# Optimization experiments

Measured on AMD Instinct MI355X. Metric: run time of the kernel, lower is better.

Reference implementation:

```python
import jax, jax.numpy as jnp
import numpy as np

PI = 3.141592653589793
TAU = 2.0      # tau for both rpe_lif (spikingjelly default 2.0) and act_conv (params['tau'])
V_TH = 1.0     # spikingjelly LIFNode default v_threshold
EPS = 1e-5     # LayerNorm / BatchNorm eps


@jax.custom_vjp
def atan_spike(x):
    # Heaviside forward, ATan surrogate backward (spikingjelly surrogate.ATan, alpha=2)
    return (x >= 0.0).astype(x.dtype)

def _atan_fwd(x):
    return atan_spike(x), x

def _atan_bwd(x, g):
    # (alpha/2) / (1 + ((pi/2)*alpha*x)^2) with alpha=2 -> 1/(1+(pi*x)^2)
    return (g / (1.0 + (PI * x) ** 2),)

atan_spike.defvjp(_atan_fwd, _atan_bwd)


def lif(x_seq, tau=TAU):
    """Multi-step LIF: decay_input=True, v_reset=0, hard reset, detach_reset.
    x_seq: [T, ...]; returns spikes [T, ...]."""
    def step(v, x):
        v = v + (x - v) / tau                      # neuronal charge
        s = atan_spike(v - V_TH)                   # fire
        v = v * (1.0 - jax.lax.stop_gradient(s))   # detached hard reset to 0
        return v, s
    _, spikes = jax.lax.scan(step, jnp.zeros_like(x_seq[0]), x_seq)
    return spikes


def setup_inputs() -> dict:
    key = jax.random.key(0)
    ks = jax.random.split(key, 8)
    B, L, D, T = 256, 50, 128, 4
    n_items, n_h, n_v = 100001, 8, 4
    emb = jax.random.normal(ks[0], (n_items, D), jnp.float32) * 0.5
    emb = emb.at[0].set(0.0)  # padding_idx=0
    return {
        "item_seq": jax.random.randint(ks[1], (B, L), 0, n_items, jnp.int32),
        "emb_table": emb,
        "ln_gamma": jnp.ones((D,), jnp.float32),
        "ln_beta": jnp.zeros((D,), jnp.float32),
        "conv_v_w": jax.random.normal(ks[2], (n_v, L), jnp.float32) * float(1.0 / np.sqrt(L)),
        # per-length kernels stored padded: kernel for length k=i+1 is conv_h_w[i, :, :k, :]
        "conv_h_w": jax.random.normal(ks[3], (L, n_h, L, D), jnp.float32) * 0.02,
        "bn_gamma": jnp.ones((L, n_h), jnp.float32),
        "bn_beta": jnp.zeros((L, n_h), jnp.float32),
        "fc_h_w": jax.random.normal(ks[4], (D, n_h * L), jnp.float32) * 0.05,
        "fc_h_b": jnp.zeros((D,), jnp.float32),
        "fc_v_w": jax.random.normal(ks[5], (D, n_v * D), jnp.float32) * 0.04,
        "fc_v_b": jnp.zeros((D,), jnp.float32),
        "T": 4,
    }


def reference(item_seq, emb_table, ln_gamma, ln_beta, conv_v_w, conv_h_w,
              bn_gamma, bn_beta, fc_h_w, fc_h_b, fc_v_w, fc_v_b, T):
    B, L = item_seq.shape
    D = emb_table.shape[1]
    n_h = conv_h_w.shape[1]
    n_v = conv_v_w.shape[0]

    # embedding + LayerNorm
    emb = emb_table[item_seq]                                   # [B,L,D]
    mu = emb.mean(-1, keepdims=True)
    var = emb.var(-1, keepdims=True)
    x = (emb - mu) / jnp.sqrt(var + EPS) * ln_gamma + ln_beta   # [B,L,D]

    # repeat over T and spike (rpe_lif)
    s = lif(jnp.broadcast_to(x, (T, B, L, D)))                  # binary spikes [T,B,L,D]

    # vertical conv: kernel (L,1), no bias -> collapses seq axis
    out_v = jnp.einsum('tbld,cl->tbcd', s, conv_v_w).reshape(T, B, n_v * D)

    # horizontal multi-scale convs + BN(train stats) + LIF + global max pool
    s2 = s.reshape(T * B, 1, L, D)
    pools = []
    for i in range(L):
        k = i + 1
        w = conv_h_w[i, :, :k, :][:, None]                      # [n_h,1,k,D]
        y = jax.lax.conv_general_dilated(
            s2, w, (1, 1), 'VALID',
            dimension_numbers=('NCHW', 'OIHW', 'NCHW'))[:, :, :, 0]  # [TB,n_h,L-k+1]
        m = y.mean(axis=(0, 2))                                  # BN over (T*B, spatial)
        v = y.var(axis=(0, 2))
        y = (y - m[:, None]) * (bn_gamma[i][:, None] / jnp.sqrt(v[:, None] + EPS)) + bn_beta[i][:, None]
        y = lif(y.reshape(T, B, n_h, L - k + 1))                 # [T,B,n_h,L-k+1]
        pools.append(y.max(axis=-1))                             # [T,B,n_h]
    out_h = jnp.concatenate(pools, axis=-1)                      # [T,B,n_h*L]

    out_h = (out_h @ fc_h_w.T + fc_h_b).mean(0)                  # [B,D]
    out_v = out_v.mean(0) @ fc_v_w.T + fc_v_b                    # [B,D]
    return out_h + out_v
```

## Files before the change

### kernel.cpp

```cpp
#include <hip/hip_runtime.h>

#define B_ 256
#define L_ 50
#define D_ 128
#define T_ 4
#define NH 8
#define NV 4
#define TB_ (T_*B_)
#define EPSF 1e-5f

typedef _Float16 h8 __attribute__((ext_vector_type(8)));
typedef float f4 __attribute__((ext_vector_type(4)));

typedef __attribute__((address_space(1))) const unsigned int gas_u32;
typedef __attribute__((address_space(3))) unsigned int las_u32;
#define GLOAD_LDS16(gp, lp) __builtin_amdgcn_global_load_lds((gas_u32*)(gp), (las_u32*)(lp), 16, 0, 0)

__device__ __forceinline__ float waveSum(float v) {
    #pragma unroll
    for (int o = 32; o > 0; o >>= 1) v += __shfl_down(v, o, 64);
    return v;
}

__device__ __forceinline__ size_t yoff(int i) {
    return (size_t)8192 * (size_t)(50 * i - (i * (i - 1)) / 2);
}

__global__ __launch_bounds__(256) void k0_wsplit(
        const float* __restrict__ w, _Float16* __restrict__ whl) {
    int dk = blockIdx.x, i = blockIdx.y;
    int t = threadIdx.x;
    int c = t >> 4, gd = t & 15;
    int h = c & 7;
    bool live = (i < 50) && (dk <= i);
    const float* src = w + (((size_t)i * NH + h) * L_ + dk) * D_ + gd * 8;
    h8 o;
    #pragma unroll
    for (int e = 0; e < 8; ++e) {
        float wv = live ? src[e] : 0.f;
        _Float16 hi = (_Float16)wv;
        o[e] = (c < 8) ? hi : (_Float16)((wv - (float)hi) * 1024.f);
    }
    *(h8*)(whl + (((size_t)i * 50 + dk) * 16 + c) * 128 + ((gd ^ c) & 15) * 8) = o;
}

__global__ __launch_bounds__(128) void k1_embed_ln_lif(
        const int* __restrict__ item, const float* __restrict__ tab,
        const float* __restrict__ g, const float* __restrict__ be,
        _Float16* __restrict__ s16, float* __restrict__ smean) {
    int bid = blockIdx.x;
    int b = bid / L_, l = bid % L_;
    int d = threadIdx.x;
    int wid = d >> 6, lane = d & 63;
    __shared__ float red[2];
    int it = item[b * L_ + l];
    float e = tab[(size_t)it * D_ + d];
    float sm_ = waveSum(e);
    if (lane == 0) red[wid] = sm_;
    __syncthreads();
    float mu = (red[0] + red[1]) * (1.f / 128.f);
    __syncthreads();
    float df = e - mu;
    float s2 = waveSum(df * df);
    if (lane == 0) red[wid] = s2;
    __syncthreads();
    float var = (red[0] + red[1]) * (1.f / 128.f);
    float x = df / sqrtf(var + EPSF) * g[d] + be[d];
    float v = 0.f, acc = 0.f;
    int pos = (((d >> 3) ^ l) & 15) * 8 + (d & 7);
    #pragma unroll
    for (int t = 0; t < T_; ++t) {
        v += (x - v) * 0.5f;
        float sp = (v >= 1.f) ? 1.f : 0.f;
        v *= (1.f - sp);
        s16[((size_t)(t * B_ + b) * L_ + l) * D_ + pos] = (_Float16)sp;
        acc += sp;
    }
    smean[((size_t)b * L_ + l) * D_ + d] = acc * 0.25f;
}

template<int MTG>
__global__ __launch_bounds__(256, 1) void k2a(
        const _Float16* __restrict__ s16, const _Float16* __restrict__ whl,
        float* __restrict__ y, int gbase) {
    extern __shared__ __align__(16) char lds[];
    char* bring = lds + 51200;
    const int tbq = blockIdx.x;
    const int grp = gbase + blockIdx.y;
    const int i0 = grp * 4;
    const int kmax = i0 + 4;
    const int tid = threadIdx.x;
    const int wave = tid >> 6, lane = tid & 63;
    const int c_ = lane & 15, g = lane >> 4;

    {
        const float4* src = (const float4*)(s16 + (size_t)tbq * 4 * (L_ * D_));
        float4* dst = (float4*)lds;
        for (int idx = tid; idx < 3200; idx += 256) dst[idx] = src[idx];
    }
    const char* bsrc = (const char*)(whl + ((size_t)(i0 + wave) * 50) * 2048);
    {
        #pragma unroll
        for (int s = 0; s < 5; ++s) {
            if (s < kmax) {
                const char* gp = bsrc + (size_t)s * 4096 + lane * 16;
                char* lp = bring + s * 16384 + wave * 4096 + lane * 16;
                #pragma unroll
                for (int q = 0; q < 4; ++q)
                    GLOAD_LDS16(gp + q * 1024, lp + q * 1024);
            }
        }
    }
    asm volatile("s_waitcnt lgkmcnt(0)" ::: "memory");
    __builtin_amdgcn_s_barrier();
    __builtin_amdgcn_sched_barrier(0);

    f4 acc[4][MTG];
    #pragma unroll
    for (int s = 0; s < 4; ++s)
        #pragma unroll
        for (int j = 0; j < MTG; ++j) { f4 z = {0.f, 0.f, 0.f, 0.f}; acc[s][j] = z; }

    const char* Abase = lds + wave * 12800;
    int boff[4];
    #pragma unroll
    for (int dc = 0; dc < 4; ++dc)
        boff[dc] = c_ * 256 + ((((dc << 2) + g) ^ c_) & 15) * 16;

    int rdpos = 0, wrpos = 81920;
    for (int dk = 0; dk < kmax; ++dk) {
        int ahead = kmax - 1 - dk; if (ahead > 4) ahead = 4;
        if (ahead >= 4)      asm volatile("s_waitcnt vmcnt(16)" ::: "memory");
        else if (ahead == 3) asm volatile("s_waitcnt vmcnt(12)" ::: "memory");
        else if (ahead == 2) asm volatile("s_waitcnt vmcnt(8)" ::: "memory");
        else if (ahead == 1) asm volatile("s_waitcnt vmcnt(4)" ::: "memory");
        else                 asm volatile("s_waitcnt vmcnt(0)" ::: "memory");
        __builtin_amdgcn_s_barrier();
        __builtin_amdgcn_sched_barrier(0);
        if (dk + 5 < kmax) {
            const char* gp = bsrc + (size_t)(dk + 5) * 4096 + lane * 16;
            char* lp = bring + wrpos + wave * 4096 + lane * 16;
            #pragma unroll
            for (int q = 0; q < 4; ++q)
                GLOAD_LDS16(gp + q * 1024, lp + q * 1024);
        }
        const char* Bs = bring + rdpos;
        #pragma unroll
        for (int dc = 0; dc < 4; ++dc) {
            h8 b0 = *(const h8*)(Bs + boff[dc]);
            h8 b1 = *(const h8*)(Bs + 4096 + boff[dc]);
            h8 b2 = *(const h8*)(Bs + 8192 + boff[dc]);
            h8 b3 = *(const h8*)(Bs + 12288 + boff[dc]);
            #pragma unroll
            for (int jt = 0; jt < MTG; ++jt) {
                int l = jt * 16 + c_ + dk; if (l > 49) l = 49;
                h8 a = *(const h8*)(Abase + l * 256 + ((((dc << 2) + g) ^ l) & 15) * 16);
                acc[0][jt] = __builtin_amdgcn_mfma_f32_16x16x32_f16(a, b0, acc[0][jt], 0, 0, 0);
                acc[1][jt] = __builtin_amdgcn_mfma_f32_16x16x32_f16(a, b1, acc[1][jt], 0, 0, 0);
                acc[2][jt] = __builtin_amdgcn_mfma_f32_16x16x32_f16(a, b2, acc[2][jt], 0, 0, 0);
                acc[3][jt] = __builtin_amdgcn_mfma_f32_16x16x32_f16(a, b3, acc[3][jt], 0, 0, 0);
            }
        }
        rdpos += 16384; if (rdpos == 98304) rdpos = 0;
        wrpos += 16384; if (wrpos == 98304) wrpos = 0;
    }
    const int tb = tbq * 4 + wave;
    const bool hiLane = (c_ < 8);
    const int h = c_ & 7;
    #pragma unroll
    for (int s = 0; s < 4; ++s) {
        const int i = i0 + s;
        const int J = 50 - i;
        size_t yb = yoff(i) + ((size_t)tb * NH + h) * J;
        #pragma unroll
        for (int jt = 0; jt < MTG; ++jt) {
            #pragma unroll
            for (int r = 0; r < 4; ++r) {
                float lo = __shfl_xor(acc[s][jt][r], 8, 64);
                int j = jt * 16 + g * 4 + r;
                if (hiLane && j < J) y[yb + j] = acc[s][jt][r] + lo * (1.f / 1024.f);
            }
        }
    }
}

__global__ __launch_bounds__(256, 1) void k2c(
        const _Float16* __restrict__ s16, const _Float16* __restrict__ whl,
        float* __restrict__ y) {
    extern __shared__ __align__(16) char lds[];
    char* bring = lds + 102400;
    const int tbo = blockIdx.x;
    const int i0 = 36 + blockIdx.y * 4;
    const int kmax = (i0 + 4 <= 50) ? (i0 + 4) : 50;
    const int tid = threadIdx.x;
    const int wave = tid >> 6, lane = tid & 63;
    const int tq = wave & 1, sg = wave >> 1;
    const int c_ = lane & 15, g = lane >> 4;

    {
        const float4* src = (const float4*)(s16 + (size_t)tbo * 8 * (L_ * D_));
        float4* dst = (float4*)lds;
        for (int idx = tid; idx < 6400; idx += 256) dst[idx] = src[idx];
    }
    const char* bsrc = (const char*)(whl + ((size_t)(i0 + wave) * 50) * 2048);
    {
        #pragma unroll
        for (int s = 0; s < 2; ++s) {
            const char* gp = bsrc + (size_t)s * 4096 + lane * 16;
            char* lp = bring + s * 16384 + wave * 4096 + lane * 16;
            #pragma unroll
            for (int q = 0; q < 4; ++q)
                GLOAD_LDS16(gp + q * 1024, lp + q * 1024);
        }
    }
    asm volatile("s_waitcnt lgkmcnt(0)" ::: "memory");
    __builtin_amdgcn_s_barrier();
    __builtin_amdgcn_sched_barrier(0);

    f4 acc[2][4];
    #pragma unroll
    for (int s = 0; s < 2; ++s)
        #pragma unroll
        for (int t = 0; t < 4; ++t) { f4 z = {0.f, 0.f, 0.f, 0.f}; acc[s][t] = z; }

    const char* Aq = lds + (tq * 4) * 12800;
    int boff[4];
    #pragma unroll
    for (int dc = 0; dc < 4; ++dc)
        boff[dc] = c_ * 256 + ((((dc << 2) + g) ^ c_) & 15) * 16;

    int rdpos = 0, wrpos = 32768;
    for (int dk = 0; dk < kmax; ++dk) {
        if (dk + 1 < kmax) asm volatile("s_waitcnt vmcnt(4)" ::: "memory");
        else               asm volatile("s_waitcnt vmcnt(0)" ::: "memory");
        __builtin_amdgcn_s_barrier();
        __builtin_amdgcn_sched_barrier(0);
        if (dk + 2 < kmax) {
            const char* gp = bsrc + (size_t)(dk + 2) * 4096 + lane * 16;
            char* lp = bring + wrpos + wave * 4096 + lane * 16;
            #pragma unroll
            for (int q = 0; q < 4; ++q)
                GLOAD_LDS16(gp + q * 1024, lp + q * 1024);
        }
        const char* Bs = bring + rdpos + sg * 8192;
        #pragma unroll
        for (int dc = 0; dc < 4; ++dc) {
            h8 b0 = *(const h8*)(Bs + boff[dc]);
            h8 b1 = *(const h8*)(Bs + 4096 + boff[dc]);
            int l = c_ + dk; if (l > 49) l = 49;
            int aoff = l * 256 + ((((dc << 2) + g) ^ l) & 15) * 16;
            #pragma unroll
            for (int tbL = 0; tbL < 4; ++tbL) {
                h8 a = *(const h8*)(Aq + tbL * 12800 + aoff);
                acc[0][tbL] = __builtin_amdgcn_mfma_f32_16x16x32_f16(a, b0, acc[0][tbL], 0, 0, 0);
                acc[1][tbL] = __builtin_amdgcn_mfma_f32_16x16x32_f16(a, b1, acc[1][tbL], 0, 0, 0);
            }
        }
        rdpos += 16384; if (rdpos == 49152) rdpos = 0;
        wrpos += 16384; if (wrpos == 49152) wrpos = 0;
    }
    const bool hiLane = (c_ < 8);
    const int h = c_ & 7;
    #pragma unroll
    for (int s = 0; s < 2; ++s) {
        const int i = i0 + sg * 2 + s;
        const int J = 50 - i;
        if (J <= 0) continue;
        #pragma unroll
        for (int tbL = 0; tbL < 4; ++tbL) {
            const int tb = tbo * 8 + tq * 4 + tbL;
            size_t yb = yoff(i) + ((size_t)tb * NH + h) * J;
            #pragma unroll
            for (int r = 0; r < 4; ++r) {
                float lo = __shfl_xor(acc[s][tbL][r], 8, 64);
                int j = g * 4 + r;
                if (hiLane && j < J) y[yb + j] = acc[s][tbL][r] + lo * (1.f / 1024.f);
            }
        }
    }
}

__global__ __launch_bounds__(256) void k3_partial(
        const float* __restrict__ y, float* __restrict__ psum) {
    int ih = blockIdx.x, ck = blockIdx.y;
    int i = ih >> 3, h = ih & 7;
    int J = 50 - i;
    size_t yb = yoff(i);
    int tid = threadIdx.x;
    int grp = tid >> 5, sub = tid & 31;
    float sm = 0.f, ss = 0.f;
    for (int tb = ck * 128 + grp; tb < (ck + 1) * 128; tb += 8) {
        const float* row = y + yb + ((size_t)tb * NH + h) * J;
        for (int j = sub; j < J; j += 32) { float v = row[j]; sm += v; ss += v * v; }
    }
    __shared__ float r1[4], r2[4];
    float a = waveSum(sm), b = waveSum(ss);
    int wid = tid >> 6, lane = tid & 63;
    if (lane == 0) { r1[wid] = a; r2[wid] = b; }
    __syncthreads();
    if (tid == 0) {
        psum[((size_t)ih * 8 + ck) * 2]     = r1[0] + r1[1] + r1[2] + r1[3];
        psum[((size_t)ih * 8 + ck) * 2 + 1] = r2[0] + r2[1] + r2[2] + r2[3];
    }
}

__global__ __launch_bounds__(256) void k3_final(
        const float* __restrict__ psum, const float* __restrict__ bng,
        float* __restrict__ statm, float* __restrict__ stats_) {
    int ih = blockIdx.x * 256 + threadIdx.x;
    if (ih >= 400) return;
    float S = 0.f, Q = 0.f;
    for (int ck = 0; ck < 8; ++ck) {
        S += psum[((size_t)ih * 8 + ck) * 2];
        Q += psum[((size_t)ih * 8 + ck) * 2 + 1];
    }
    int i = ih >> 3;
    float cnt = 1024.f * (float)(50 - i);
    float m = S / cnt;
    float var = Q / cnt - m * m; if (var < 0.f) var = 0.f;
    statm[ih] = m;
    stats_[ih] = bng[ih] / sqrtf(var + EPSF);
}

__global__ __launch_bounds__(512) void k4_bn_lif_pool(
        const float* __restrict__ y, const float* __restrict__ statm,
        const float* __restrict__ stats_, const float* __restrict__ bnb,
        float* __restrict__ ps) {
    int b = blockIdx.x, i = blockIdx.y, J = L_ - i;
    int h = threadIdx.x >> 6, lane = threadIdx.x & 63;
    int ih = i * NH + h;
    float m = statm[ih], sc = stats_[ih], bb = bnb[ih];
    size_t yb = yoff(i);
    bool valid = lane < J;
    float v = 0.f; int cnt = 0;
    #pragma unroll
    for (int t = 0; t < T_; ++t) {
        int tb = t * B_ + b;
        float yn;
        if (valid) {
            float raw = y[yb + ((size_t)tb * NH + h) * J + lane];
            yn = (raw - m) * sc + bb;
        } else yn = -1e30f;
        v += (yn - v) * 0.5f;
        bool sp = (v >= 1.f);
        if (sp) v = 0.f;
        if (__any(sp)) cnt++;
    }
    if (lane == 0) ps[(size_t)b * 400 + ih] = (float)cnt;
}

__global__ __launch_bounds__(128) void k5_final(
        const float* __restrict__ smean, const float* __restrict__ ps,
        const float* __restrict__ convv, const float* __restrict__ fchw,
        const float* __restrict__ fchb, const float* __restrict__ fcvw,
        const float* __restrict__ fcvb, float* __restrict__ out) {
    __shared__ float sm_l[L_ * D_];
    __shared__ float vm[NV * D_];
    __shared__ float ps_l[400];
    int b = blockIdx.x, tid = threadIdx.x;
    for (int idx = tid; idx < L_ * D_; idx += 128) sm_l[idx] = smean[(size_t)b * (L_ * D_) + idx];
    for (int idx = tid; idx < 400; idx += 128) ps_l[idx] = ps[(size_t)b * 400 + idx];
    __syncthreads();
    int d = tid;
    #pragma unroll
    for (int c = 0; c < NV; ++c) {
        float a = 0.f;
        for (int l = 0; l < L_; ++l) a += convv[c * L_ + l] * sm_l[l * D_ + d];
        vm[c * D_ + d] = a;
    }
    __syncthreads();
    float acc = fchb[d] + fcvb[d];
    float ah = 0.f;
    for (int ih = 0; ih < 400; ++ih) ah += ps_l[ih] * fchw[d * 400 + ih];
    acc += ah * 0.25f;
    float av = 0.f;
    for (int cd = 0; cd < NV * D_; ++cd) av += vm[cd] * fcvw[d * (NV * D_) + cd];
    acc += av;
    out[(size_t)b * D_ + d] = acc;
}

extern "C" void kernel_launch(void* const* d_in, const int* in_sizes, int n_in,
                              void* d_out, int out_size, void* d_ws, size_t ws_size,
                              hipStream_t stream) {
    const int*   item  = (const int*)d_in[0];
    const float* tab   = (const float*)d_in[1];
    const float* lng   = (const float*)d_in[2];
    const float* lnb   = (const float*)d_in[3];
    const float* convv = (const float*)d_in[4];
    const float* convh = (const float*)d_in[5];
    const float* bng   = (const float*)d_in[6];
    const float* bnb   = (const float*)d_in[7];
    const float* fchw  = (const float*)d_in[8];
    const float* fchb  = (const float*)d_in[9];
    const float* fcvw  = (const float*)d_in[10];
    const float* fcvb  = (const float*)d_in[11];
    float* out = (float*)d_out;

    char* ws = (char*)d_ws;
    _Float16* s16  = (_Float16*)(ws);
    float* smean   = (float*)(ws + 13107200LL);
    float* y       = (float*)(ws + 19660800LL);
    _Float16* whl  = (_Float16*)(ws + 61440000LL);
    float* statm   = (float*)(ws + 72089600LL);
    float* stats_  = (float*)(ws + 72091200LL);
    float* ps      = (float*)(ws + 72092800LL);
    float* psum    = (float*)(ws + 72502400LL);

    hipFuncSetAttribute(reinterpret_cast<const void*>(&k2a<4>),
        hipFuncAttributeMaxDynamicSharedMemorySize, 149504);
    hipFuncSetAttribute(reinterpret_cast<const void*>(&k2a<3>),
        hipFuncAttributeMaxDynamicSharedMemorySize, 149504);
    hipFuncSetAttribute(reinterpret_cast<const void*>(&k2a<2>),
        hipFuncAttributeMaxDynamicSharedMemorySize, 149504);
    hipFuncSetAttribute(reinterpret_cast<const void*>(&k2c),
        hipFuncAttributeMaxDynamicSharedMemorySize, 151552);

    k0_wsplit<<<dim3(50, 52), 256, 0, stream>>>(convh, whl);
    k1_embed_ln_lif<<<B_ * L_, 128, 0, stream>>>(item, tab, lng, lnb, s16, smean);
    k2a<4><<<dim3(256, 1), 256, 149504, stream>>>(s16, whl, y, 0);
    k2a<3><<<dim3(256, 4), 256, 149504, stream>>>(s16, whl, y, 1);
    k2a<2><<<dim3(256, 4), 256, 149504, stream>>>(s16, whl, y, 5);
    k2c<<<dim3(128, 4), 256, 151552, stream>>>(s16, whl, y);
    k3_partial<<<dim3(400, 8), 256, 0, stream>>>(y, psum);
    k3_final<<<dim3(2, 1), 256, 0, stream>>>(psum, bng, statm, stats_);
    k4_bn_lif_pool<<<dim3(B_, L_), 512, 0, stream>>>(y, statm, stats_, bnb, ps);
    k5_final<<<B_, 128, 0, stream>>>(smean, ps, convv, fchw, fchb, fcvw, fcvb, out);
}
```

Measured before the change: 336.2 us.

## Restructure horizontal conv GEMM to share B tiles across 8 batch rows with split-K waves

The k2a kernels are replaced by k2u, which uses 512 threads per block over 8 TB rows instead of 4. Each block loads a single shared 16KB weight slab for all four scales, replacing the per-wave 5-deep global_load_lds ring. The four D-chunks are split between wave pairs, and their partial accumulators are reduced through LDS at the end. Weights are register-prefetched one step ahead and written into a single LDS slot between two barriers. This halves global weight traffic per row and cuts LDS use so two blocks can fit per CU. The costs are two barriers per step, shallower prefetch, and a final cross-wave reduction.

```diff
diff --git a/kernel.cpp b/kernel.cpp
--- a/kernel.cpp
+++ b/kernel.cpp
@@ -80,105 +80,126 @@
 }
 
 template<int MTG>
-__global__ __launch_bounds__(256, 1) void k2a(
+__global__ __launch_bounds__(512, 2) void k2u(
         const _Float16* __restrict__ s16, const _Float16* __restrict__ whl,
         float* __restrict__ y, int gbase) {
     extern __shared__ __align__(16) char lds[];
-    char* bring = lds + 51200;
-    const int tbq = blockIdx.x;
+    char* Bslot = lds + 102400;
+    const int NM = 2 * MTG;
+    const int tbo = blockIdx.x;
     const int grp = gbase + blockIdx.y;
     const int i0 = grp * 4;
     const int kmax = i0 + 4;
     const int tid = threadIdx.x;
     const int wave = tid >> 6, lane = tid & 63;
+    const int p = wave >> 1;
+    const int dh = wave & 1;
     const int c_ = lane & 15, g = lane >> 4;
 
     {
-        const float4* src = (const float4*)(s16 + (size_t)tbq * 4 * (L_ * D_));
+        const float4* src = (const float4*)(s16 + (size_t)tbo * 8 * (L_ * D_));
         float4* dst = (float4*)lds;
-        for (int idx = tid; idx < 3200; idx += 256) dst[idx] = src[idx];
-    }
-    const char* bsrc = (const char*)(whl + ((size_t)(i0 + wave) * 50) * 2048);
-    {
-        #pragma unroll
-        for (int s = 0; s < 5; ++s) {
-            if (s < kmax) {
-                const char* gp = bsrc + (size_t)s * 4096 + lane * 16;
-                char* lp = bring + s * 16384 + wave * 4096 + lane * 16;
+        for (int idx = tid; idx < 6400; idx += 512) dst[idx] = src[idx];
+    }
+    const char* bsrc = (const char*)whl + (size_t)i0 * 50 * 4096;
+    const int o0 = tid * 16, o1 = 8192 + tid * 16;
+    const int sc0 = o0 >> 12, r0 = o0 & 4095;
+    const int sc1 = o1 >> 12, r1 = o1 & 4095;
+    const char* g0p = bsrc + (size_t)sc0 * (50 * 4096) + r0;
+    const char* g1p = bsrc + (size_t)sc1 * (50 * 4096) + r1;
+
+    float4 n0 = *(const float4*)(g0p);
+    float4 n1 = *(const float4*)(g1p);
+    __syncthreads();
+    *(float4*)(Bslot + o0) = n0;
+    *(float4*)(Bslot + o1) = n1;
+    __syncthreads();
+
+    f4 acc[4][NM];
+    #pragma unroll
+    for (int sc = 0; sc < 4; ++sc)
+        #pragma unroll
+        for (int m = 0; m < NM; ++m) { f4 z = {0.f, 0.f, 0.f, 0.f}; acc[sc][m] = z; }
+
+    for (int dk = 0; dk < kmax; ++dk) {
+        const bool more = (dk + 1 < kmax);
+        float4 m0, m1;
+        if (more) {
+            m0 = *(const float4*)(g0p + (size_t)(dk + 1) * 4096);
+            m1 = *(const float4*)(g1p + (size_t)(dk + 1) * 4096);
+        }
+        __builtin_amdgcn_sched_barrier(0);
+        #pragma unroll
+        for (int dci = 0; dci < 2; ++dci) {
+            const int dc = dh * 2 + dci;
+            h8 bf[4];
+            #pragma unroll
+            for (int sc = 0; sc < 4; ++sc)
+                bf[sc] = *(const h8*)(Bslot + sc * 4096 + c_ * 256 +
+                                      ((((dc << 2) + g) ^ c_) & 15) * 16);
+            #pragma unroll
+            for (int m = 0; m < NM; ++m) {
+                const int tbL = p * 2 + (m >= MTG ? 1 : 0);
+                const int jt = (m >= MTG) ? m - MTG : m;
+                int l = jt * 16 + c_ + dk; if (l > 49) l = 49;
+                h8 a = *(const h8*)(lds + tbL * 12800 + l * 256 +
+                                    ((((dc << 2) + g) ^ l) & 15) * 16);
                 #pragma unroll
-                for (int q = 0; q < 4; ++q)
-                    GLOAD_LDS16(gp + q * 1024, lp + q * 1024);
+                for (int sc = 0; sc < 4; ++sc)
+                    acc[sc][m] = __builtin_amdgcn_mfma_f32_16x16x32_f16(a, bf[sc], acc[sc][m], 0, 0, 0);
             }
         }
-    }
-    asm volatile("s_waitcnt lgkmcnt(0)" ::: "memory");
-    __builtin_amdgcn_s_barrier();
-    __builtin_amdgcn_sched_barrier(0);
-
-    f4 acc[4][MTG];
-    #pragma unroll
-    for (int s = 0; s < 4; ++s)
-        #pragma unroll
-        for (int j = 0; j < MTG; ++j) { f4 z = {0.f, 0.f, 0.f, 0.f}; acc[s][j] = z; }
-
-    const char* Abase = lds + wave * 12800;
-    int boff[4];
-    #pragma unroll
-    for (int dc = 0; dc < 4; ++dc)
-        boff[dc] = c_ * 256 + ((((dc << 2) + g) ^ c_) & 15) * 16;
-
-    int rdpos = 0, wrpos = 81920;
-    for (int dk = 0; dk < kmax; ++dk) {
-        int ahead = kmax - 1 - dk; if (ahead > 4) ahead = 4;
-        if (ahead >= 4)      asm volatile("s_waitcnt vmcnt(16)" ::: "memory");
-        else if (ahead == 3) asm volatile("s_waitcnt vmcnt(12)" ::: "memory");
-        else if (ahead == 2) asm volatile("s_waitcnt vmcnt(8)" ::: "memory");
-        else if (ahead == 1) asm volatile("s_waitcnt vmcnt(4)" ::: "memory");
-        else                 asm volatile("s_waitcnt vmcnt(0)" ::: "memory");
-        __builtin_amdgcn_s_barrier();
-        __builtin_amdgcn_sched_barrier(0);
-        if (dk + 5 < kmax) {
-            const char* gp = bsrc + (size_t)(dk + 5) * 4096 + lane * 16;
-            char* lp = bring + wrpos + wave * 4096 + lane * 16;
-            #pragma unroll
-            for (int q = 0; q < 4; ++q)
-                GLOAD_LDS16(gp + q * 1024, lp + q * 1024);
-        }
-        const char* Bs = bring + rdpos;
-        #pragma unroll
-        for (int dc = 0; dc < 4; ++dc) {
-            h8 b0 = *(const h8*)(Bs + boff[dc]);
-            h8 b1 = *(const h8*)(Bs + 4096 + boff[dc]);
-            h8 b2 = *(const h8*)(Bs + 8192 + boff[dc]);
-            h8 b3 = *(const h8*)(Bs + 12288 + boff[dc]);
-            #pragma unroll
-            for (int jt = 0; jt < MTG; ++jt) {
-                int l = jt * 16 + c_ + dk; if (l > 49) l = 49;
-                h8 a = *(const h8*)(Abase + l * 256 + ((((dc << 2) + g) ^ l) & 15) * 16);
-                acc[0][jt] = __builtin_amdgcn_mfma_f32_16x16x32_f16(a, b0, acc[0][jt], 0, 0, 0);
-                acc[1][jt] = __builtin_amdgcn_mfma_f32_16x16x32_f16(a, b1, acc[1][jt], 0, 0, 0);
-                acc[2][jt] = __builtin_amdgcn_mfma_f32_16x16x32_f16(a, b2, acc[2][jt], 0, 0, 0);
-                acc[3][jt] = __builtin_amdgcn_mfma_f32_16x16x32_f16(a, b3, acc[3][jt], 0, 0, 0);
-            }
-        }
-        rdpos += 16384; if (rdpos == 98304) rdpos = 0;
-        wrpos += 16384; if (wrpos == 98304) wrpos = 0;
-    }
-    const int tb = tbq * 4 + wave;
-    const bool hiLane = (c_ < 8);
-    const int h = c_ & 7;
-    #pragma unroll
-    for (int s = 0; s < 4; ++s) {
-        const int i = i0 + s;
-        const int J = 50 - i;
-        size_t yb = yoff(i) + ((size_t)tb * NH + h) * J;
-        #pragma unroll
-        for (int jt = 0; jt < MTG; ++jt) {
-            #pragma unroll
-            for (int r = 0; r < 4; ++r) {
-                float lo = __shfl_xor(acc[s][jt][r], 8, 64);
-                int j = jt * 16 + g * 4 + r;
-                if (hiLane && j < J) y[yb + j] = acc[s][jt][r] + lo * (1.f / 1024.f);
+        __syncthreads();
+        if (more) {
+            *(float4*)(Bslot + o0) = m0;
+            *(float4*)(Bslot + o1) = m1;
+        }
+        __syncthreads();
+    }
+
+    const int STR = 2 * NM * 4 + 4;
+    float* mbuf = (float*)lds;
+    #pragma unroll
+    for (int half = 0; half < 2; ++half) {
+        __syncthreads();
+        if (dh == 1) {
+            float* wp = mbuf + (size_t)(p * 64 + lane) * STR;
+            #pragma unroll
+            for (int sc = 0; sc < 2; ++sc)
+                #pragma unroll
+                for (int m = 0; m < NM; ++m)
+                    *(f4*)(wp + (sc * NM + m) * 4) = acc[2 * half + sc][m];
+        }
+        __syncthreads();
+        if (dh == 0) {
+            const float* rp = mbuf + (size_t)(p * 64 + lane) * STR;
+            #pragma unroll
+            for (int sc = 0; sc < 2; ++sc)
+                #pragma unroll
+                for (int m = 0; m < NM; ++m)
+                    acc[2 * half + sc][m] += *(const f4*)(rp + (sc * NM + m) * 4);
+        }
+    }
+
+    if (dh == 0) {
+        const bool hiLane = (c_ < 8);
+        const int h = c_ & 7;
+        #pragma unroll
+        for (int sc = 0; sc < 4; ++sc) {
+            const int i = i0 + sc;
+            const int J = 50 - i;
+            #pragma unroll
+            for (int m = 0; m < NM; ++m) {
+                const int tbL = p * 2 + (m >= MTG ? 1 : 0);
+                const int jt = (m >= MTG) ? m - MTG : m;
+                const int tb = tbo * 8 + tbL;
+                size_t yb = yoff(i) + ((size_t)tb * NH + h) * J;
+                #pragma unroll
+                for (int r = 0; r < 4; ++r) {
+                    float lo = __shfl_xor(acc[sc][m][r], 8, 64);
+                    int j = jt * 16 + g * 4 + r;
+                    if (hiLane && j < J) y[yb + j] = acc[sc][m][r] + lo * (1.f / 1024.f);
+                }
             }
         }
     }
@@ -406,20 +427,20 @@
     float* ps      = (float*)(ws + 72092800LL);
     float* psum    = (float*)(ws + 72502400LL);
 
-    hipFuncSetAttribute(reinterpret_cast<const void*>(&k2a<4>),
-        hipFuncAttributeMaxDynamicSharedMemorySize, 149504);
-    hipFuncSetAttribute(reinterpret_cast<const void*>(&k2a<3>),
-        hipFuncAttributeMaxDynamicSharedMemorySize, 149504);
-    hipFuncSetAttribute(reinterpret_cast<const void*>(&k2a<2>),
-        hipFuncAttributeMaxDynamicSharedMemorySize, 149504);
+    hipFuncSetAttribute(reinterpret_cast<const void*>(&k2u<4>),
+        hipFuncAttributeMaxDynamicSharedMemorySize, 118784);
+    hipFuncSetAttribute(reinterpret_cast<const void*>(&k2u<3>),
+        hipFuncAttributeMaxDynamicSharedMemorySize, 118784);
+    hipFuncSetAttribute(reinterpret_cast<const void*>(&k2u<2>),
+        hipFuncAttributeMaxDynamicSharedMemorySize, 118784);
     hipFuncSetAttribute(reinterpret_cast<const void*>(&k2c),
         hipFuncAttributeMaxDynamicSharedMemorySize, 151552);
 
     k0_wsplit<<<dim3(50, 52), 256, 0, stream>>>(convh, whl);
     k1_embed_ln_lif<<<B_ * L_, 128, 0, stream>>>(item, tab, lng, lnb, s16, smean);
-    k2a<4><<<dim3(256, 1), 256, 149504, stream>>>(s16, whl, y, 0);
-    k2a<3><<<dim3(256, 4), 256, 149504, stream>>>(s16, whl, y, 1);
-    k2a<2><<<dim3(256, 4), 256, 149504, stream>>>(s16, whl, y, 5);
+    k2u<4><<<dim3(128, 1), 512, 118784, stream>>>(s16, whl, y, 0);
+    k2u<3><<<dim3(128, 4), 512, 118784, stream>>>(s16, whl, y, 1);
+    k2u<2><<<dim3(128, 4), 512, 118784, stream>>>(s16, whl, y, 5);
     k2c<<<dim3(128, 4), 256, 151552, stream>>>(s16, whl, y);
     k3_partial<<<dim3(400, 8), 256, 0, stream>>>(y, psum);
     k3_final<<<dim3(2, 1), 256, 0, stream>>>(psum, bng, statm, stats_);
```

Result: faster. 290.6 us (-13.6%).
